# Kernel tuning notes

Hardware: AMD Instinct MI355X
Metric: run time of the kernel (lower is better)

Reference implementation:

```python
import math
import jax, jax.numpy as jnp
import numpy as np
from jax import lax

RADIUS = 3
KSIZE = 2 * RADIUS + 1  # 7
TOP_K = 8
SINKHORN_ITERS = 5


def _box_sum(x, h_axis, w_axis):
    # sum pooling with same padding over spatial axes
    wd = [1] * x.ndim
    wd[h_axis] = KSIZE
    wd[w_axis] = KSIZE
    pads = [(0, 0)] * x.ndim
    pads[h_axis] = (RADIUS, RADIUS)
    pads[w_axis] = (RADIUS, RADIUS)
    return lax.reduce_window(x, 0.0, lax.add, tuple(wd), (1,) * x.ndim, pads)


def geo_validate(src_pos, cand_pos, H, W):
    # src_pos [B,N,2], cand_pos [B,N,K,2] -> score [B,N,K]
    B, N, K, _ = cand_pos.shape
    src = src_pos.reshape(B, H, W, 1, 2)
    cand = cand_pos.reshape(B, H, W, K, 2)
    disp = cand - src  # [B,H,W,K,2]
    # count_include_pad=False -> divide by number of valid (in-bounds) taps
    cnt = _box_sum(jnp.ones((1, H, W, 1, 1), disp.dtype), 1, 2)
    mean = _box_sum(disp, 1, 2) / cnt
    mean_sq = _box_sum(disp * disp, 1, 2) / cnt
    var = jnp.clip(mean_sq - mean * mean, 0.0)
    total_var = var.sum(-1).reshape(B, N, K)
    return 1.0 / (1.0 + 100.0 * total_var)


def optimal_transport(scores, dustbin):
    B, M, N = scores.shape
    row = jnp.broadcast_to(dustbin, (B, M, 1))
    col = jnp.broadcast_to(dustbin, (B, 1, N))
    corner = jnp.zeros((B, 1, 1), scores.dtype)
    Z = jnp.concatenate([jnp.concatenate([scores, row], 2),
                         jnp.concatenate([col, corner], 2)], 1)  # [B,M+1,N+1]
    norm = -math.log(M + N)
    log_mu = jnp.full((M + 1,), norm, scores.dtype).at[M].set(math.log(N) + norm)
    log_nu = jnp.full((N + 1,), norm, scores.dtype).at[N].set(math.log(M) + norm)
    log_mu = jnp.broadcast_to(log_mu, (B, M + 1))
    log_nu = jnp.broadcast_to(log_nu, (B, N + 1))

    def body(_, uv):
        u, v = uv
        u = log_mu - jax.nn.logsumexp(Z + v[:, None, :], axis=2)
        v = log_nu - jax.nn.logsumexp(Z + u[:, :, None], axis=1)
        return (u, v)

    u0 = jnp.zeros((B, M + 1), scores.dtype)
    v0 = jnp.zeros((B, N + 1), scores.dtype)
    u, v = lax.fori_loop(0, SINKHORN_ITERS, body, (u0, v0))
    log_assign = Z + u[:, :, None] + v[:, None, :]
    return log_assign[:, :M, :N]


def solve_weighted_affine(src_pts, dst_pts, weights):
    # src/dst [B,N,2], weights [B,N,1] -> H_mat [B,3,3]
    B, N, _ = src_pts.shape
    w = weights[..., 0]
    w = w / jnp.clip(w.sum(1, keepdims=True), 1e-6)
    x, y = src_pts[..., 0], src_pts[..., 1]
    one = jnp.ones_like(x)
    zero = jnp.zeros_like(x)
    row_x = jnp.stack([x, y, one, zero, zero, zero], -1)   # [B,N,6]
    row_y = jnp.stack([zero, zero, zero, x, y, one], -1)
    A = jnp.concatenate([row_x, row_y], 1)                 # [B,2N,6]
    b = jnp.concatenate([dst_pts[..., 0], dst_pts[..., 1]], 1)[..., None]
    wd = jnp.concatenate([w, w], 1)[..., None]             # [B,2N,1]
    Aw = A * wd
    AtWA = jnp.einsum('bni,bnj->bij', Aw, A) + 1e-4 * jnp.eye(6, dtype=A.dtype)
    AtWb = jnp.einsum('bni,bnk->bik', Aw, b)
    p = jnp.linalg.solve(AtWA, AtWb)[..., 0]               # [B,6]
    a_, b_, c_, d_, e_, f_ = [p[:, i] for i in range(6)]
    z = jnp.zeros_like(a_)
    o = jnp.ones_like(a_)
    return jnp.stack([a_, b_, c_, d_, e_, f_, z, z, o], -1).reshape(B, 3, 3)


def matcher_forward(feat_A, feat_B, pos_A, pos_B, dustbin_score, geo_weight,
                    current_temp, H, W):
    B, N, C = feat_A.shape
    temp = current_temp[0]
    nA = feat_A / jnp.clip(jnp.linalg.norm(feat_A, axis=-1, keepdims=True), 1e-12)
    nB = feat_B / jnp.clip(jnp.linalg.norm(feat_B, axis=-1, keepdims=True), 1e-12)
    scores = jnp.einsum('bnc,bmc->bnm', nA, nB) / temp      # [B,N,N]
    log_assign = optimal_transport(scores, dustbin_score[0])
    ot_prob = jnp.exp(log_assign)
    topk_vals, topk_idx = lax.top_k(ot_prob, TOP_K)          # [B,N,K]
    bidx = jnp.arange(B)[:, None, None]
    topk_pos = pos_B[bidx, topk_idx]                         # [B,N,K,2]
    geo = geo_validate(pos_A, topk_pos, H, W)                # [B,N,K]
    gw = jnp.clip(geo_weight[0], 0.0, 2.0)
    combined = topk_vals + gw * geo
    soft = jax.nn.softmax(combined / temp, axis=-1)
    refined_warp = (topk_pos * soft[..., None]).sum(2)       # [B,N,2]
    conf = (soft * topk_vals).sum(-1, keepdims=True)         # [B,N,1]
    H_mat = solve_weighted_affine(pos_A, refined_warp, conf)
    return refined_warp, conf, H_mat


def setup_inputs() -> dict:
    key = jax.random.key(0)
    kA, kB, kP = jax.random.split(key, 3)
    B, H, W, C = 2, 64, 64, 128
    N = H * W
    feat_A = jax.random.normal(kA, (B, N, C), jnp.float32)
    feat_B = jax.random.normal(kB, (B, N, C), jnp.float32)
    # dense grid positions, normalized to [0,1]
    ys, xs = jnp.meshgrid(jnp.arange(H, dtype=jnp.float32),
                          jnp.arange(W, dtype=jnp.float32), indexing='ij')
    grid = jnp.stack([xs, ys], -1).reshape(1, N, 2) / float(max(H, W))
    pos_A = jnp.broadcast_to(grid, (B, N, 2))
    pos_B = pos_A + 0.01 * jax.random.normal(kP, (B, N, 2), jnp.float32)
    return {
        'feat_A': feat_A, 'feat_B': feat_B,
        'pos_A': pos_A, 'pos_B': pos_B,
        'dustbin_score': jnp.full((1,), -1.0, jnp.float32),
        'geo_weight': jnp.full((1,), 0.5, jnp.float32),
        'current_temp': jnp.full((1,), 0.1, jnp.float32),
        'H': H, 'W': W,
    }


def reference(feat_A, feat_B, pos_A, pos_B, dustbin_score, geo_weight,
              current_temp, H, W):
    return matcher_forward(feat_A, feat_B, pos_A, pos_B, dustbin_score,
                           geo_weight, current_temp, H, W)
```

## Files before the change

kernel.cpp:

```cpp
#include <hip/hip_runtime.h>
#include <math.h>

#define UVS 4104

#define OFF_ZU    33554432ul
#define OFF_WV    (OFF_ZU + 2*UVS)
#define OFF_RN    (OFF_WV + 2*UVS)
#define OFF_PARTS (OFF_RN + 16384)
#define OFF_TKV   (OFF_PARTS + 2097152)
#define OFF_TKP   (OFF_TKV + 65536)
#define OFF_DP    (OFF_TKP + 131072)
#define OFF_GEO   (OFF_DP + 131072)
#define OFF_SUM   (OFF_GEO + 65536)

#define EXPC    0.0001220703125f
#define HALFC   0.5f

#define PLANE   1048576

typedef __attribute__((ext_vector_type(8))) short bf16x8;
typedef __attribute__((ext_vector_type(4))) float f32x4;

static __device__ __forceinline__ unsigned f2bf(float x) {
    unsigned u = __float_as_uint(x);
    return (u + 0x7FFFu + ((u >> 16) & 1u)) >> 16;
}
static __device__ __forceinline__ float bf2f(unsigned h) { return __uint_as_float(h << 16); }

static __device__ __forceinline__ unsigned long long shfl_xor_u64(unsigned long long v, int m) {
    unsigned lo = (unsigned)v, hi = (unsigned)(v >> 32);
    lo = __shfl_xor(lo, m, 64);
    hi = __shfl_xor(hi, m, 64);
    return ((unsigned long long)hi << 32) | lo;
}

__global__ __launch_bounds__(256) void init_kernel(float* __restrict__ wv)
{
    int i = blockIdx.x * 256 + threadIdx.x;
    if (i < 2 * UVS) wv[i] = 1.0f;
}

__global__ __launch_bounds__(256) void norms_kernel(
    const float* __restrict__ fA, const float* __restrict__ fB, float* __restrict__ rn)
{
    int t = threadIdx.x;
    int rowg = blockIdx.x * 4 + (t >> 6);
    int lane = t & 63;
    const float* f = (rowg < 8192) ? fA : fB;
    int r = rowg & 8191;
    float x0 = f[(size_t)r * 128 + lane];
    float x1 = f[(size_t)r * 128 + 64 + lane];
    float s = x0 * x0 + x1 * x1;
    #pragma unroll
    for (int off = 32; off > 0; off >>= 1) s += __shfl_xor(s, off, 64);
    if (lane == 0) rn[rowg] = 1.f / fmaxf(sqrtf(s), 1e-12f);
}

__global__ __launch_bounds__(256) void pack_kernel(
    const float* __restrict__ fA, const float* __restrict__ fB, short* __restrict__ pk)
{
    int gt = blockIdx.x * 256 + threadIdx.x;
    int tensor = gt >> 17;
    int t = gt & 131071;
    int fr = t & 15;
    int kc = (t >> 4) & 15;
    int rb = (t >> 8) & 255;
    int b  = t >> 16;
    const float* src = tensor ? fB : fA;
    const float* p = src + ((size_t)(b * 4096 + rb * 16 + fr)) * 128 + kc * 8;
    float4 v0 = *(const float4*)p;
    float4 v1 = *(const float4*)(p + 4);
    float el[8] = {v0.x, v0.y, v0.z, v0.w, v1.x, v1.y, v1.z, v1.w};
    unsigned h[8], l[8];
    #pragma unroll
    for (int e = 0; e < 8; e++) { h[e] = f2bf(el[e]); l[e] = f2bf(el[e] - bf2f(h[e])); }
    uint4 hw = make_uint4(h[0] | (h[1] << 16), h[2] | (h[3] << 16),
                          h[4] | (h[5] << 16), h[6] | (h[7] << 16));
    uint4 lw = make_uint4(l[0] | (l[1] << 16), l[2] | (l[3] << 16),
                          l[4] | (l[5] << 16), l[6] | (l[7] << 16));
    size_t off = ((size_t)(b * 256 + rb)) * 2048 + kc * 128 + fr * 8;
    short* hi = pk + (size_t)tensor * 2 * PLANE;
    *(uint4*)(hi + off) = hw;
    *(uint4*)(hi + PLANE + off) = lw;
}

__global__ __launch_bounds__(256) void gemm_mfma(
    const short* __restrict__ pk, const float* __restrict__ rn,
    const float* __restrict__ temp, float* __restrict__ E0)
{
    __shared__ short Bs[16384];
    int b = blockIdx.z;
    int i0 = blockIdx.y * 64, j0 = blockIdx.x * 64;
    int t = threadIdx.x;
    int wave = t >> 6, lane = t & 63;
    int fr = lane & 15;
    int quad = lane >> 4;

    const short* gBhi = pk + 2 * (size_t)PLANE + ((size_t)(b * 256 + (j0 >> 4))) * 2048;
    const short* gBlo = gBhi + PLANE;
    #pragma unroll
    for (int c = 0; c < 4; c++) {
        int ch = c * 256 + t;
        *(uint4*)&Bs[ch * 8]        = *(const uint4*)(gBhi + ch * 8);
        *(uint4*)&Bs[8192 + ch * 8] = *(const uint4*)(gBlo + ch * 8);
    }

    const short* Abase_hi = pk + ((size_t)(b * 256 + (i0 >> 4) + wave)) * 2048;
    const short* Abase_lo = Abase_hi + PLANE;
    bf16x8 ah[4], al[4];
    #pragma unroll
    for (int s = 0; s < 4; s++) {
        ah[s] = *(const bf16x8*)(Abase_hi + s * 512 + lane * 8);
        al[s] = *(const bf16x8*)(Abase_lo + s * 512 + lane * 8);
    }
    __syncthreads();

    f32x4 acc[4] = {f32x4{0,0,0,0}, f32x4{0,0,0,0}, f32x4{0,0,0,0}, f32x4{0,0,0,0}};
    #pragma unroll
    for (int s = 0; s < 4; s++) {
        int lo = s * 512 + lane * 8;
        #pragma unroll
        for (int nb = 0; nb < 4; nb++) {
            bf16x8 bh = *(const bf16x8*)&Bs[nb * 2048 + lo];
            bf16x8 bl = *(const bf16x8*)&Bs[8192 + nb * 2048 + lo];
            acc[nb] = __builtin_amdgcn_mfma_f32_16x16x32_bf16(ah[s], bh, acc[nb], 0, 0, 0);
            acc[nb] = __builtin_amdgcn_mfma_f32_16x16x32_bf16(al[s], bh, acc[nb], 0, 0, 0);
            acc[nb] = __builtin_amdgcn_mfma_f32_16x16x32_bf16(ah[s], bl, acc[nb], 0, 0, 0);
        }
    }

    float invt = 1.f / temp[0];
    int m0 = i0 + wave * 16 + quad * 4;
    float ra[4];
    #pragma unroll
    for (int rr = 0; rr < 4; rr++) ra[rr] = rn[b * 4096 + m0 + rr] * invt;
    #pragma unroll
    for (int nb = 0; nb < 4; nb++) {
        int col = j0 + nb * 16 + fr;
        float rbv = rn[8192 + b * 4096 + col];
        #pragma unroll
        for (int rr = 0; rr < 4; rr++)
            E0[((size_t)(b * 4096 + m0 + rr)) * 4096 + col] = __expf(acc[nb][rr] * (ra[rr] * rbv));
    }
}

__global__ __launch_bounds__(256) void sink_fused(
    const float* __restrict__ E0, float* __restrict__ zu, const float* __restrict__ wv,
    const float* __restrict__ dbp, float* __restrict__ parts)
{
    int b = blockIdx.z;
    int ch = blockIdx.x;
    int t = threadIdx.x;
    int wave = t >> 6, lane = t & 63;
    const float* wb = wv + b * UVS;
    float edb = __expf(dbp[0]);
    __shared__ float Sch[4 * 4096];
    __shared__ float z4[4];

    if (ch == 0) {
        __shared__ float red[256];
        float sv = 0.f;
        #pragma unroll
        for (int k = 0; k < 16; k++) sv += wb[t + k * 256];
        red[t] = sv; __syncthreads();
        for (int off = 128; off > 0; off >>= 1) {
            if (t < off) red[t] += red[t + off];
            __syncthreads();
        }
        if (t == 0) zu[b * UVS + 4096] = HALFC / (edb * red[0] + wb[4096]);
        __syncthreads();
    }

    float dtail = edb * wb[4096];
    float colacc[16];
    #pragma unroll
    for (int k = 0; k < 16; k++) colacc[k] = 0.f;

    const float* Eb = E0 + (size_t)b * 4096 * 4096;

    for (int st = 0; st < 4; st++) {
        int row = ch * 16 + st * 4 + wave;
        const float* Erow = Eb + (size_t)row * 4096;
        float rs = 0.f;
        #pragma unroll
        for (int c = 0; c < 16; c++) {
            int j = lane * 4 + c * 256;
            float4 x = *(const float4*)(Erow + j);
            float4 w = *(const float4*)(wb + j);
            float4 q = make_float4(x.x * w.x, x.y * w.y, x.z * w.z, x.w * w.w);
            *(float4*)&Sch[wave * 4096 + j] = q;
            rs += (q.x + q.y) + (q.z + q.w);
        }
        #pragma unroll
        for (int off = 32; off > 0; off >>= 1) rs += __shfl_xor(rs, off, 64);
        if (lane == 0) {
            float zi = EXPC / (rs + dtail);
            zu[b * UVS + row] = zi;
            z4[wave] = zi;
        }
        __syncthreads();
        float z0 = z4[0], z1 = z4[1], z2 = z4[2], z3 = z4[3];
        #pragma unroll
        for (int k = 0; k < 16; k++) {
            int c = t + k * 256;
            colacc[k] += Sch[c] * z0 + Sch[4096 + c] * z1
                       + Sch[8192 + c] * z2 + Sch[12288 + c] * z3;
        }
        __syncthreads();
    }
    float* pp = parts + ((size_t)(b * 256 + ch)) * 4096;
    #pragma unroll
    for (int k = 0; k < 16; k++) pp[t + k * 256] = colacc[k];
}

__global__ __launch_bounds__(256) void sink_vB(
    const float* __restrict__ parts, const float* __restrict__ zu,
    float* __restrict__ wv, const float* __restrict__ dbp)
{
    int b = blockIdx.z;
    int t = threadIdx.x;
    float edb = __expf(dbp[0]);
    if (blockIdx.x < 16) {
        int j = blockIdx.x * 256 + t;
        float s = 0.f;
        #pragma unroll 16
        for (int ch = 0; ch < 256; ch++) s += parts[((size_t)(b * 256 + ch)) * 4096 + j];
        float wold = wv[b * UVS + j];
        float total = s / wold + edb * zu[b * UVS + 4096];
        wv[b * UVS + j] = EXPC / total;
    } else {
        __shared__ float red[256];
        float s = 0.f;
        for (int i = t; i < 4096; i += 256) s += zu[b * UVS + i];
        red[t] = s; __syncthreads();
        for (int off = 128; off > 0; off >>= 1) {
            if (t < off) red[t] += red[t + off];
            __syncthreads();
        }
        if (t == 0)
            wv[b * UVS + 4096] = HALFC / (edb * red[0] + zu[b * UVS + 4096]);
    }
}

#define CMPSWAP(a, b) { unsigned long long _mx = (a) > (b) ? (a) : (b); \
                        unsigned long long _mn = (a) > (b) ? (b) : (a); \
                        (a) = _mx; (b) = _mn; }
#define FCMPSWAP(a, b) { float _mx = fmaxf(a, b), _mn = fminf(a, b); (a) = _mx; (b) = _mn; }
__global__ __launch_bounds__(256) void topk_kernel(
    const float* __restrict__ E0, const float* __restrict__ zu, const float* __restrict__ wv,
    const float* __restrict__ posA, const float* __restrict__ posB,
    float* __restrict__ tkv, float* __restrict__ tkp, float* __restrict__ dp)
{
    int wave = threadIdx.x >> 6;
    int lane = threadIdx.x & 63;
    int row = blockIdx.x * 4 + wave;
    int b = row >> 12; int i = row & 4095;
    const float* Erow = E0 + (size_t)row * 4096;
    const float* wb = wv + b * UVS;

    __shared__ unsigned long long cand[4][64];
    __shared__ int ccnt[4];
    if (lane == 0) ccnt[wave] = 0;

    float4 q[16];
    float s[8] = {0, 0, 0, 0, 0, 0, 0, 0};
    #pragma unroll
    for (int c = 0; c < 16; c++) {
        int j = c * 256 + lane * 4;
        float4 x = *(const float4*)(Erow + j);
        float4 w = *(const float4*)(wb + j);
        q[c] = make_float4(x.x * w.x, x.y * w.y, x.z * w.z, x.w * w.w);
        float el[4] = {q[c].x, q[c].y, q[c].z, q[c].w};
        #pragma unroll
        for (int e = 0; e < 4; e++) {
            float xv = el[e];
            #pragma unroll
            for (int rr = 0; rr < 8; rr++) {
                float mx = fmaxf(s[rr], xv);
                float mn = fminf(s[rr], xv);
                s[rr] = mx; xv = mn;
            }
        }
    }

    #pragma unroll
    for (int st = 0; st < 6; st++) {
        int off = 1 << st;
        float o[8];
        #pragma unroll
        for (int r = 0; r < 8; r++) o[r] = __shfl_xor(s[r], off, 64);
        float m[8];
        #pragma unroll
        for (int r = 0; r < 8; r++) m[r] = fmaxf(s[r], o[7 - r]);
        FCMPSWAP(m[0], m[4]); FCMPSWAP(m[1], m[5]); FCMPSWAP(m[2], m[6]); FCMPSWAP(m[3], m[7]);
        FCMPSWAP(m[0], m[2]); FCMPSWAP(m[1], m[3]); FCMPSWAP(m[4], m[6]); FCMPSWAP(m[5], m[7]);
        FCMPSWAP(m[0], m[1]); FCMPSWAP(m[2], m[3]); FCMPSWAP(m[4], m[5]); FCMPSWAP(m[6], m[7]);
        #pragma unroll
        for (int r = 0; r < 8; r++) s[r] = m[r];
    }
    float t8 = s[7];

    __syncthreads();

    #pragma unroll
    for (int c = 0; c < 16; c++) {
        float el[4] = {q[c].x, q[c].y, q[c].z, q[c].w};
        #pragma unroll
        for (int e = 0; e < 4; e++) {
            if (el[e] >= t8) {
                int j = c * 256 + lane * 4 + e;
                unsigned long long key =
                    ((unsigned long long)__float_as_uint(el[e]) << 32) | (unsigned)(4095 - j);
                int slot = atomicAdd(&ccnt[wave], 1);
                if (slot < 64) cand[wave][slot] = key;
            }
        }
    }
    __syncthreads();

    int cnt = ccnt[wave]; if (cnt > 64) cnt = 64;
    unsigned long long loc[8];
    loc[0] = (lane < cnt) ? cand[wave][lane] : 0ull;
    #pragma unroll
    for (int r = 1; r < 8; r++) loc[r] = 0ull;
    #pragma unroll
    for (int st = 0; st < 6; st++) {
        int off = 1 << st;
        unsigned long long oth[8];
        #pragma unroll
        for (int r = 0; r < 8; r++) oth[r] = shfl_xor_u64(loc[r], off);
        unsigned long long m[8];
        #pragma unroll
        for (int r = 0; r < 8; r++) {
            unsigned long long a = loc[r], bb = oth[7 - r];
            m[r] = a > bb ? a : bb;
        }
        CMPSWAP(m[0], m[4]); CMPSWAP(m[1], m[5]); CMPSWAP(m[2], m[6]); CMPSWAP(m[3], m[7]);
        CMPSWAP(m[0], m[2]); CMPSWAP(m[1], m[3]); CMPSWAP(m[4], m[6]); CMPSWAP(m[5], m[7]);
        CMPSWAP(m[0], m[1]); CMPSWAP(m[2], m[3]); CMPSWAP(m[4], m[5]); CMPSWAP(m[6], m[7]);
        #pragma unroll
        for (int r = 0; r < 8; r++) loc[r] = m[r];
    }

    if (lane < 8) {
        unsigned long long key = loc[0];
        #pragma unroll
        for (int r = 1; r < 8; r++) if (lane == r) key = loc[r];
        int idx = 4095 - (int)(key & 0xFFFFFFFFu);
        float candv = __uint_as_float((unsigned)(key >> 32));
        float val = candv * zu[b * UVS + i];
        float px = posB[((size_t)(b * 4096 + idx)) * 2 + 0];
        float py = posB[((size_t)(b * 4096 + idx)) * 2 + 1];
        float ax = posA[((size_t)(b * 4096 + i)) * 2 + 0];
        float ay = posA[((size_t)(b * 4096 + i)) * 2 + 1];
        size_t base = ((size_t)(b * 4096 + i)) * 8 + lane;
        tkv[base] = val;
        tkp[base * 2 + 0] = px; tkp[base * 2 + 1] = py;
        dp[((size_t)((b * 8 + lane) * 2 + 0)) * 4096 + i] = px - ax;
        dp[((size_t)((b * 8 + lane) * 2 + 1)) * 4096 + i] = py - ay;
    }
}

__global__ __launch_bounds__(256) void geo_kernel(
    const float* __restrict__ dp, float* __restrict__ geo)
{
    int tid = blockIdx.x * 256 + threadIdx.x;
    int n = tid & 4095; int bk = tid >> 12;
    int b = bk >> 3; int k = bk & 7;
    int h = n >> 6, w = n & 63;
    const float* dpx = dp + ((size_t)(bk * 2 + 0)) * 4096;
    const float* dpy = dp + ((size_t)(bk * 2 + 1)) * 4096;
    float sx = 0, sy = 0, sxx = 0, syy = 0, cnt = 0;
    #pragma unroll
    for (int dy = -3; dy <= 3; dy++) {
        int hh = h + dy; if ((unsigned)hh >= 64u) continue;
        #pragma unroll
        for (int dx = -3; dx <= 3; dx++) {
            int ww = w + dx; if ((unsigned)ww >= 64u) continue;
            int nn = (hh << 6) + ww;
            float vx = dpx[nn], vy = dpy[nn];
            sx += vx; sy += vy; sxx += vx * vx; syy += vy * vy; cnt += 1.f;
        }
    }
    float inv = 1.f / cnt;
    float mx = sx * inv, my = sy * inv;
    float varx = fmaxf(sxx * inv - mx * mx, 0.f);
    float vary = fmaxf(syy * inv - my * my, 0.f);
    geo[((size_t)(b * 4096 + n)) * 8 + k] = 1.f / (1.f + 100.f * (varx + vary));
}

__global__ __launch_bounds__(256) void refine_kernel(
    const float* __restrict__ tkv, const float* __restrict__ geo,
    const float* __restrict__ tkp, const float* __restrict__ gwp,
    const float* __restrict__ tpp, float* __restrict__ out)
{
    int tid = blockIdx.x * 256 + threadIdx.x;
    float gw = fminf(fmaxf(gwp[0], 0.f), 2.f);
    float invt = 1.f / tpp[0];
    size_t base = (size_t)tid * 8;
    float cb[8], vv[8];
    float mx = -INFINITY;
    #pragma unroll
    for (int k = 0; k < 8; k++) { vv[k] = tkv[base + k]; cb[k] = vv[k] + gw * geo[base + k]; mx = fmaxf(mx, cb[k]); }
    float e[8], se = 0;
    #pragma unroll
    for (int k = 0; k < 8; k++) { e[k] = __expf((cb[k] - mx) * invt); se += e[k]; }
    float wx = 0, wy = 0, cf = 0; float inv = 1.f / se;
    #pragma unroll
    for (int k = 0; k < 8; k++) {
        float s = e[k] * inv;
        wx += s * tkp[(base + k) * 2 + 0];
        wy += s * tkp[(base + k) * 2 + 1];
        cf += s * vv[k];
    }
    out[(size_t)tid * 2 + 0] = wx;
    out[(size_t)tid * 2 + 1] = wy;
    out[16384 + tid] = cf;
}

__global__ __launch_bounds__(256) void affine_reduce(
    const float* __restrict__ posA, const float* __restrict__ out, double* __restrict__ sums)
{
    int b = blockIdx.x; int t = threadIdx.x;
    double acc[12] = {0,0,0,0,0,0,0,0,0,0,0,0};
    for (int n = t; n < 4096; n += 256) {
        size_t idx = (size_t)b * 4096 + n;
        float x = posA[idx * 2], y = posA[idx * 2 + 1];
        float dx = out[idx * 2], dy = out[idx * 2 + 1];
        float c = out[16384 + idx];
        double cd = (double)c;
        double cx = cd * x, cy = cd * y;
        acc[0] += cx * x;  acc[1] += cx * y;  acc[2] += cy * y;
        acc[3] += cx;      acc[4] += cy;      acc[5] += cd;
        acc[6] += cx * dx; acc[7] += cy * dx; acc[8] += cd * dx;
        acc[9] += cx * dy; acc[10] += cy * dy; acc[11] += cd * dy;
    }
    __shared__ double red[256];
    for (int s = 0; s < 12; s++) {
        red[t] = acc[s]; __syncthreads();
        for (int off = 128; off > 0; off >>= 1) {
            if (t < off) red[t] += red[t + off];
            __syncthreads();
        }
        if (t == 0) sums[b * 12 + s] = red[0];
        __syncthreads();
    }
}

__global__ void affine_solve(const double* __restrict__ sums, float* __restrict__ out)
{
    int t = threadIdx.x;
    if (t >= 2) return;
    int b = t;
    const double* s = sums + b * 12;
    double den = s[5] > 1e-6 ? s[5] : 1e-6;
    double g00 = s[0] / den + 1e-4, g01 = s[1] / den, g02 = s[3] / den;
    double g11 = s[2] / den + 1e-4, g12 = s[4] / den;
    double g22 = s[5] / den + 1e-4;
    double bx0 = s[6] / den, bx1 = s[7] / den, bx2 = s[8] / den;
    double by0 = s[9] / den, by1 = s[10] / den, by2 = s[11] / den;
    double c00 = g11 * g22 - g12 * g12;
    double c01 = g02 * g12 - g01 * g22;
    double c02 = g01 * g12 - g02 * g11;
    double det = g00 * c00 + g01 * c01 + g02 * c02;
    double id = 1.0 / det;
    double i00 = c00 * id, i01 = c01 * id, i02 = c02 * id;
    double i11 = (g00 * g22 - g02 * g02) * id, i12 = (g01 * g02 - g00 * g12) * id;
    double i22 = (g00 * g11 - g01 * g01) * id;
    double a_ = i00 * bx0 + i01 * bx1 + i02 * bx2;
    double b_ = i01 * bx0 + i11 * bx1 + i12 * bx2;
    double c_ = i02 * bx0 + i12 * bx1 + i22 * bx2;
    double d_ = i00 * by0 + i01 * by1 + i02 * by2;
    double e_ = i01 * by0 + i11 * by1 + i12 * by2;
    double f_ = i02 * by0 + i12 * by1 + i22 * by2;
    float* o = out + 24576 + b * 9;
    o[0] = (float)a_; o[1] = (float)b_; o[2] = (float)c_;
    o[3] = (float)d_; o[4] = (float)e_; o[5] = (float)f_;
    o[6] = 0.f; o[7] = 0.f; o[8] = 1.f;
}

extern "C" void kernel_launch(void* const* d_in, const int* in_sizes, int n_in,
                              void* d_out, int out_size, void* d_ws, size_t ws_size,
                              hipStream_t stream) {
    const float* fA = (const float*)d_in[0];
    const float* fB = (const float*)d_in[1];
    const float* pA = (const float*)d_in[2];
    const float* pB = (const float*)d_in[3];
    const float* db = (const float*)d_in[4];
    const float* gw = (const float*)d_in[5];
    const float* tp = (const float*)d_in[6];

    float* ws    = (float*)d_ws;
    float* out   = (float*)d_out;
    float* E0    = ws;
    float* zu    = ws + OFF_ZU;
    float* wv    = ws + OFF_WV;
    float* rn    = ws + OFF_RN;
    float* parts = ws + OFF_PARTS;
    short* pk    = (short*)(ws + OFF_PARTS);
    float* tkv   = ws + OFF_TKV;
    float* tkp   = ws + OFF_TKP;
    float* dp    = ws + OFF_DP;
    float* geo   = ws + OFF_GEO;
    double* sums = (double*)(ws + OFF_SUM);

    init_kernel<<<33, 256, 0, stream>>>(wv);
    norms_kernel<<<4096, 256, 0, stream>>>(fA, fB, rn);
    pack_kernel<<<1024, 256, 0, stream>>>(fA, fB, pk);
    gemm_mfma<<<dim3(64, 64, 2), 256, 0, stream>>>(pk, rn, tp, E0);

    for (int it = 0; it < 5; it++) {
        sink_fused<<<dim3(256, 1, 2), 256, 0, stream>>>(E0, zu, wv, db, parts);
        sink_vB<<<dim3(17, 1, 2), 256, 0, stream>>>(parts, zu, wv, db);
    }

    topk_kernel<<<2048, 256, 0, stream>>>(E0, zu, wv, pA, pB, tkv, tkp, dp);
    geo_kernel<<<256, 256, 0, stream>>>(dp, geo);
    refine_kernel<<<32, 256, 0, stream>>>(tkv, geo, tkp, gw, tp, out);
    affine_reduce<<<2, 256, 0, stream>>>(pA, out, sums);
    affine_solve<<<1, 64, 0, stream>>>(sums, out);
}
```

Measured before the change: 368.7 us.

## Make Sinkhorn row chunks per-wave, drop LDS staging; simplify top-k with med3 and rank

The fused Sinkhorn kernel now gives each wave its own 16-row chunk and keeps the row in registers. Column partials accumulate directly from E0 times the row scale, with no shared-memory staging and no block barriers. The partials now omit the column weight, so the column update no longer divides by the old weight. The top-k kernel swaps the max/min insertion network for fmed3, reloads rows instead of keeping 16 float4 in registers, and replaces the 64-bit bitonic wave merge with a rank count over the candidate list. This trades register pressure and syncs for re-reading E0 rows once more from cache or memory.

```diff
diff --git a/kernel.cpp b/kernel.cpp
--- a/kernel.cpp
+++ b/kernel.cpp
@@ -26,13 +26,6 @@
     return (u + 0x7FFFu + ((u >> 16) & 1u)) >> 16;
 }
 static __device__ __forceinline__ float bf2f(unsigned h) { return __uint_as_float(h << 16); }
-
-static __device__ __forceinline__ unsigned long long shfl_xor_u64(unsigned long long v, int m) {
-    unsigned lo = (unsigned)v, hi = (unsigned)(v >> 32);
-    lo = __shfl_xor(lo, m, 64);
-    hi = __shfl_xor(hi, m, 64);
-    return ((unsigned long long)hi << 32) | lo;
-}
 
 __global__ __launch_bounds__(256) void init_kernel(float* __restrict__ wv)
 {
@@ -149,68 +142,56 @@
     const float* __restrict__ dbp, float* __restrict__ parts)
 {
     int b = blockIdx.z;
-    int ch = blockIdx.x;
     int t = threadIdx.x;
     int wave = t >> 6, lane = t & 63;
+    int ch = blockIdx.x * 4 + wave;
     const float* wb = wv + b * UVS;
     float edb = __expf(dbp[0]);
-    __shared__ float Sch[4 * 4096];
-    __shared__ float z4[4];
 
     if (ch == 0) {
-        __shared__ float red[256];
         float sv = 0.f;
         #pragma unroll
-        for (int k = 0; k < 16; k++) sv += wb[t + k * 256];
-        red[t] = sv; __syncthreads();
-        for (int off = 128; off > 0; off >>= 1) {
-            if (t < off) red[t] += red[t + off];
-            __syncthreads();
-        }
-        if (t == 0) zu[b * UVS + 4096] = HALFC / (edb * red[0] + wb[4096]);
-        __syncthreads();
+        for (int c = 0; c < 16; c++) {
+            f32x4 w4 = *(const f32x4*)(wb + lane * 4 + c * 256);
+            sv += (w4.x + w4.y) + (w4.z + w4.w);
+        }
+        #pragma unroll
+        for (int off = 32; off > 0; off >>= 1) sv += __shfl_xor(sv, off, 64);
+        if (lane == 0) zu[b * UVS + 4096] = HALFC / (edb * sv + wb[4096]);
     }
 
     float dtail = edb * wb[4096];
-    float colacc[16];
-    #pragma unroll
-    for (int k = 0; k < 16; k++) colacc[k] = 0.f;
-
-    const float* Eb = E0 + (size_t)b * 4096 * 4096;
-
-    for (int st = 0; st < 4; st++) {
-        int row = ch * 16 + st * 4 + wave;
-        const float* Erow = Eb + (size_t)row * 4096;
-        float rs = 0.f;
+    f32x4 cacc[16];
+    #pragma unroll
+    for (int c = 0; c < 16; c++) cacc[c] = f32x4{0, 0, 0, 0};
+
+    const float* Eb = E0 + ((size_t)b << 24);
+    int base = lane * 4;
+
+    for (int r = 0; r < 16; r++) {
+        int row = ch * 16 + r;
+        const float* Erow = Eb + ((size_t)row << 12);
+        f32x4 x4[16];
+        #pragma unroll
+        for (int c = 0; c < 16; c++) x4[c] = *(const f32x4*)(Erow + base + c * 256);
+        f32x4 rs4 = f32x4{0, 0, 0, 0};
         #pragma unroll
         for (int c = 0; c < 16; c++) {
-            int j = lane * 4 + c * 256;
-            float4 x = *(const float4*)(Erow + j);
-            float4 w = *(const float4*)(wb + j);
-            float4 q = make_float4(x.x * w.x, x.y * w.y, x.z * w.z, x.w * w.w);
-            *(float4*)&Sch[wave * 4096 + j] = q;
-            rs += (q.x + q.y) + (q.z + q.w);
-        }
+            f32x4 w4 = *(const f32x4*)(wb + base + c * 256);
+            rs4 += x4[c] * w4;
+        }
+        float rs = (rs4.x + rs4.y) + (rs4.z + rs4.w);
         #pragma unroll
         for (int off = 32; off > 0; off >>= 1) rs += __shfl_xor(rs, off, 64);
-        if (lane == 0) {
-            float zi = EXPC / (rs + dtail);
-            zu[b * UVS + row] = zi;
-            z4[wave] = zi;
-        }
-        __syncthreads();
-        float z0 = z4[0], z1 = z4[1], z2 = z4[2], z3 = z4[3];
-        #pragma unroll
-        for (int k = 0; k < 16; k++) {
-            int c = t + k * 256;
-            colacc[k] += Sch[c] * z0 + Sch[4096 + c] * z1
-                       + Sch[8192 + c] * z2 + Sch[12288 + c] * z3;
-        }
-        __syncthreads();
-    }
+        float zi = EXPC / (rs + dtail);
+        if (lane == 0) zu[b * UVS + row] = zi;
+        #pragma unroll
+        for (int c = 0; c < 16; c++) cacc[c] += x4[c] * zi;
+    }
+
     float* pp = parts + ((size_t)(b * 256 + ch)) * 4096;
     #pragma unroll
-    for (int k = 0; k < 16; k++) pp[t + k * 256] = colacc[k];
+    for (int c = 0; c < 16; c++) *(f32x4*)(pp + base + c * 256) = cacc[c];
 }
 
 __global__ __launch_bounds__(256) void sink_vB(
@@ -225,8 +206,7 @@
         float s = 0.f;
         #pragma unroll 16
         for (int ch = 0; ch < 256; ch++) s += parts[((size_t)(b * 256 + ch)) * 4096 + j];
-        float wold = wv[b * UVS + j];
-        float total = s / wold + edb * zu[b * UVS + 4096];
+        float total = s + edb * zu[b * UVS + 4096];
         wv[b * UVS + j] = EXPC / total;
     } else {
         __shared__ float red[256];
@@ -242,9 +222,6 @@
     }
 }
 
-#define CMPSWAP(a, b) { unsigned long long _mx = (a) > (b) ? (a) : (b); \
-                        unsigned long long _mn = (a) > (b) ? (b) : (a); \
-                        (a) = _mx; (b) = _mn; }
 #define FCMPSWAP(a, b) { float _mx = fmaxf(a, b), _mn = fminf(a, b); (a) = _mx; (b) = _mn; }
 __global__ __launch_bounds__(256) void topk_kernel(
     const float* __restrict__ E0, const float* __restrict__ zu, const float* __restrict__ wv,
@@ -262,24 +239,25 @@
     __shared__ int ccnt[4];
     if (lane == 0) ccnt[wave] = 0;
 
-    float4 q[16];
     float s[8] = {0, 0, 0, 0, 0, 0, 0, 0};
     #pragma unroll
     for (int c = 0; c < 16; c++) {
         int j = c * 256 + lane * 4;
-        float4 x = *(const float4*)(Erow + j);
-        float4 w = *(const float4*)(wb + j);
-        q[c] = make_float4(x.x * w.x, x.y * w.y, x.z * w.z, x.w * w.w);
-        float el[4] = {q[c].x, q[c].y, q[c].z, q[c].w};
+        f32x4 x = *(const f32x4*)(Erow + j);
+        f32x4 w = *(const f32x4*)(wb + j);
+        f32x4 q = x * w;
+        float el[4] = {q.x, q.y, q.z, q.w};
         #pragma unroll
         for (int e = 0; e < 4; e++) {
             float xv = el[e];
-            #pragma unroll
-            for (int rr = 0; rr < 8; rr++) {
-                float mx = fmaxf(s[rr], xv);
-                float mn = fminf(s[rr], xv);
-                s[rr] = mx; xv = mn;
-            }
+            s[7] = __builtin_amdgcn_fmed3f(s[6], s[7], xv);
+            s[6] = __builtin_amdgcn_fmed3f(s[5], s[6], xv);
+            s[5] = __builtin_amdgcn_fmed3f(s[4], s[5], xv);
+            s[4] = __builtin_amdgcn_fmed3f(s[3], s[4], xv);
+            s[3] = __builtin_amdgcn_fmed3f(s[2], s[3], xv);
+            s[2] = __builtin_amdgcn_fmed3f(s[1], s[2], xv);
+            s[1] = __builtin_amdgcn_fmed3f(s[0], s[1], xv);
+            s[0] = fmaxf(s[0], xv);
         }
     }
 
@@ -304,13 +282,16 @@
 
     #pragma unroll
     for (int c = 0; c < 16; c++) {
-        float el[4] = {q[c].x, q[c].y, q[c].z, q[c].w};
+        int j = c * 256 + lane * 4;
+        f32x4 x = *(const f32x4*)(Erow + j);
+        f32x4 w = *(const f32x4*)(wb + j);
+        f32x4 q = x * w;
+        float el[4] = {q.x, q.y, q.z, q.w};
         #pragma unroll
         for (int e = 0; e < 4; e++) {
             if (el[e] >= t8) {
-                int j = c * 256 + lane * 4 + e;
                 unsigned long long key =
-                    ((unsigned long long)__float_as_uint(el[e]) << 32) | (unsigned)(4095 - j);
+                    ((unsigned long long)__float_as_uint(el[e]) << 32) | (unsigned)(4095 - (j + e));
                 int slot = atomicAdd(&ccnt[wave], 1);
                 if (slot < 64) cand[wave][slot] = key;
             }
@@ -319,45 +300,24 @@
     __syncthreads();
 
     int cnt = ccnt[wave]; if (cnt > 64) cnt = 64;
-    unsigned long long loc[8];
-    loc[0] = (lane < cnt) ? cand[wave][lane] : 0ull;
-    #pragma unroll
-    for (int r = 1; r < 8; r++) loc[r] = 0ull;
-    #pragma unroll
-    for (int st = 0; st < 6; st++) {
-        int off = 1 << st;
-        unsigned long long oth[8];
-        #pragma unroll
-        for (int r = 0; r < 8; r++) oth[r] = shfl_xor_u64(loc[r], off);
-        unsigned long long m[8];
-        #pragma unroll
-        for (int r = 0; r < 8; r++) {
-            unsigned long long a = loc[r], bb = oth[7 - r];
-            m[r] = a > bb ? a : bb;
-        }
-        CMPSWAP(m[0], m[4]); CMPSWAP(m[1], m[5]); CMPSWAP(m[2], m[6]); CMPSWAP(m[3], m[7]);
-        CMPSWAP(m[0], m[2]); CMPSWAP(m[1], m[3]); CMPSWAP(m[4], m[6]); CMPSWAP(m[5], m[7]);
-        CMPSWAP(m[0], m[1]); CMPSWAP(m[2], m[3]); CMPSWAP(m[4], m[5]); CMPSWAP(m[6], m[7]);
-        #pragma unroll
-        for (int r = 0; r < 8; r++) loc[r] = m[r];
-    }
-
-    if (lane < 8) {
-        unsigned long long key = loc[0];
-        #pragma unroll
-        for (int r = 1; r < 8; r++) if (lane == r) key = loc[r];
-        int idx = 4095 - (int)(key & 0xFFFFFFFFu);
-        float candv = __uint_as_float((unsigned)(key >> 32));
-        float val = candv * zu[b * UVS + i];
-        float px = posB[((size_t)(b * 4096 + idx)) * 2 + 0];
-        float py = posB[((size_t)(b * 4096 + idx)) * 2 + 1];
-        float ax = posA[((size_t)(b * 4096 + i)) * 2 + 0];
-        float ay = posA[((size_t)(b * 4096 + i)) * 2 + 1];
-        size_t base = ((size_t)(b * 4096 + i)) * 8 + lane;
-        tkv[base] = val;
-        tkp[base * 2 + 0] = px; tkp[base * 2 + 1] = py;
-        dp[((size_t)((b * 8 + lane) * 2 + 0)) * 4096 + i] = px - ax;
-        dp[((size_t)((b * 8 + lane) * 2 + 1)) * 4096 + i] = py - ay;
+    if (lane < cnt) {
+        unsigned long long my = cand[wave][lane];
+        int rank = 0;
+        for (int j2 = 0; j2 < cnt; j2++) rank += (cand[wave][j2] > my) ? 1 : 0;
+        if (rank < 8) {
+            int idx = 4095 - (int)(my & 0xFFFFFFFFu);
+            float candv = __uint_as_float((unsigned)(my >> 32));
+            float val = candv * zu[b * UVS + i];
+            float px = posB[((size_t)(b * 4096 + idx)) * 2 + 0];
+            float py = posB[((size_t)(b * 4096 + idx)) * 2 + 1];
+            float ax = posA[((size_t)(b * 4096 + i)) * 2 + 0];
+            float ay = posA[((size_t)(b * 4096 + i)) * 2 + 1];
+            size_t base = ((size_t)(b * 4096 + i)) * 8 + rank;
+            tkv[base] = val;
+            tkp[base * 2 + 0] = px; tkp[base * 2 + 1] = py;
+            dp[((size_t)((b * 8 + rank) * 2 + 0)) * 4096 + i] = px - ax;
+            dp[((size_t)((b * 8 + rank) * 2 + 1)) * 4096 + i] = py - ay;
+        }
     }
 }
 
@@ -510,7 +470,7 @@
     gemm_mfma<<<dim3(64, 64, 2), 256, 0, stream>>>(pk, rn, tp, E0);
 
     for (int it = 0; it < 5; it++) {
-        sink_fused<<<dim3(256, 1, 2), 256, 0, stream>>>(E0, zu, wv, db, parts);
+        sink_fused<<<dim3(64, 1, 2), 256, 0, stream>>>(E0, zu, wv, db, parts);
         sink_vB<<<dim3(17, 1, 2), 256, 0, stream>>>(parts, zu, wv, db);
     }
 
```

New measurement: 359.0 us. 1.03x faster.
